# Optimization experiments

Measured on AMD Instinct MI355X. Metric: run time of the kernel, lower is better.

Reference implementation:

```python
import jax, jax.numpy as jnp
import numpy as np

B, N, FA, FP, C = 64, 64, 75, 14, 128


def _mlp2(x, W0, b0, W1, b1):
    # two lazy-Linear + ReLU sub-layers (n_sub_layer=2)
    h = jax.nn.relu(x @ W0 + b0)
    return jax.nn.relu(h @ W1 + b1)


def setup_inputs() -> dict:
    key = jax.random.key(0)
    ks = jax.random.split(key, 32)
    w = lambda k, s: jax.random.normal(k, s, jnp.float32) * 0.05
    inp = {
        "atom_x": jax.random.normal(ks[0], (B, N, FA), jnp.float32),
        "pair_x": jax.random.normal(ks[1], (B, N * N, FP), jnp.float32),
        # atom_to_atom: FA -> C -> C
        "a2a_W0": w(ks[2], (FA, C)), "a2a_b0": w(ks[3], (C,)),
        "a2a_W1": w(ks[4], (C, C)), "a2a_b1": w(ks[5], (C,)),
        # pair_to_atom: FP -> C -> C
        "p2a_W0": w(ks[6], (FP, C)), "p2a_b0": w(ks[7], (C,)),
        "p2a_W1": w(ks[8], (C, C)), "p2a_b1": w(ks[9], (C,)),
        # atom_layer: 2C -> C -> C
        "al_W0": w(ks[10], (2 * C, C)), "al_b0": w(ks[11], (C,)),
        "al_W1": w(ks[12], (C, C)), "al_b1": w(ks[13], (C,)),
        # atom_to_pair (weights shared across both orderings): 2FA -> C -> C
        "a2p_W0": w(ks[14], (2 * FA, C)), "a2p_b0": w(ks[15], (C,)),
        "a2p_W1": w(ks[16], (C, C)), "a2p_b1": w(ks[17], (C,)),
        # pair_to_pair: FP -> C -> C
        "p2p_W0": w(ks[18], (FP, C)), "p2p_b0": w(ks[19], (C,)),
        "p2p_W1": w(ks[20], (C, C)), "p2p_b1": w(ks[21], (C,)),
        # pair_layer: 2C -> C -> C
        "pl_W0": w(ks[22], (2 * C, C)), "pl_b0": w(ks[23], (C,)),
        "pl_W1": w(ks[24], (C, C)), "pl_b1": w(ks[25], (C,)),
    }
    return inp


def reference(atom_x, pair_x,
              a2a_W0, a2a_b0, a2a_W1, a2a_b1,
              p2a_W0, p2a_b0, p2a_W1, p2a_b1,
              al_W0, al_b0, al_W1, al_b1,
              a2p_W0, a2p_b0, a2p_W1, a2p_b1,
              p2p_W0, p2p_b0, p2p_W1, p2p_b1,
              pl_W0, pl_b0, pl_W1, pl_b1):
    b, n, fa = atom_x.shape
    # --- atom branch ---
    a0 = _mlp2(atom_x, a2a_W0, a2a_b0, a2a_W1, a2a_b1)            # [B,N,C]
    a1 = _mlp2(pair_x, p2a_W0, p2a_b0, p2a_W1, p2a_b1)            # [B,N*N,C]
    a1 = a1.reshape(b, n, n, -1).sum(axis=2)                      # PairToAtom sum
    a = jnp.concatenate([a0, a1], axis=-1)                        # [B,N,2C]
    next_atom = jax.nn.relu(_mlp2(a, al_W0, al_b0, al_W1, al_b1))  # extra relu per forward
    # --- pair branch ---
    rep = jnp.broadcast_to(atom_x[:, None, :, :], (b, n, n, fa))  # atom_repeat
    til = jnp.broadcast_to(atom_x[:, :, None, :], (b, n, n, fa))  # atom_tile
    pr0 = jnp.concatenate([til, rep], axis=-1).reshape(b, n * n, 2 * fa)
    pr1 = jnp.concatenate([rep, til], axis=-1).reshape(b, n * n, 2 * fa)
    p0 = (_mlp2(pr0, a2p_W0, a2p_b0, a2p_W1, a2p_b1)
          + _mlp2(pr1, a2p_W0, a2p_b0, a2p_W1, a2p_b1))            # [B,N*N,C]
    p1 = _mlp2(pair_x, p2p_W0, p2p_b0, p2p_W1, p2p_b1)            # [B,N*N,C]
    p = jnp.concatenate([p0, p1], axis=-1)                        # [B,N*N,2C]
    next_pair = jax.nn.relu(_mlp2(p, pl_W0, pl_b0, pl_W1, pl_b1))
    return (next_atom, next_pair)
```

## Files before the change

### kernel.cpp

```cpp
#include <hip/hip_runtime.h>
#include <hip/hip_bf16.h>

typedef unsigned short u16;
typedef unsigned int u32;
typedef __attribute__((ext_vector_type(8))) __bf16 bf16x8;
typedef __attribute__((ext_vector_type(4))) float f32x4;

#define B_ 64
#define N_ 64
#define FA_ 75
#define FP_ 14
#define C_ 128

__device__ float g_A0[4096 * 128];
__device__ float g_A1[4096 * 128];
__device__ float g_TB[4096 * 256];
__device__ u16   g_Wf[208896];

#define OFF_AA0   0
#define OFF_AA1   12288
#define OFF_APT   28672
#define OFF_APB   40960
#define OFF_PA0   53248
#define OFF_PA1   57344
#define OFF_AL0   73728
#define OFF_AL1   106496
#define OFF_AP1   122880
#define OFF_PP0   139264
#define OFF_PP1   143360
#define OFF_PL0T  159744
#define OFF_PL0B  176128
#define OFF_PL1   192512

__device__ __forceinline__ float bf2f(u16 a) {
    union { u32 u; float f; } v; v.u = ((u32)a) << 16; return v.f;
}
__device__ __forceinline__ u16 f2bf(float f) {
    union { float f; u32 u; } v; v.f = f;
    u32 r = v.u + 0x7fffu + ((v.u >> 16) & 1u);
    return (u16)(r >> 16);
}
#if __has_builtin(__builtin_amdgcn_cvt_pk_bf16_f32)
__device__ __forceinline__ u32 f2bf_pk(float a, float b) {
    auto r = __builtin_amdgcn_cvt_pk_bf16_f32(a, b);
    if constexpr (sizeof(r) == 4) {
        union { decltype(r) v; u32 u; } c; c.v = r; return c.u;
    } else {
        return (u32)f2bf(a) | ((u32)f2bf(b) << 16);
    }
}
#else
__device__ __forceinline__ u32 f2bf_pk(float a, float b) {
    return (u32)f2bf(a) | ((u32)f2bf(b) << 16);
}
#endif

__device__ __forceinline__ bool detect_isbf(const void* __restrict__ atom) {
    u32 wrd = ((const u32*)atom)[threadIdx.x & 63];
    u32 ex = (wrd >> 7) & 0xffu;
    unsigned long long m = __ballot(ex >= 113u && ex <= 133u);
    return __popcll(m) >= 32;
}

__device__ __forceinline__ float ldf(const void* p, size_t i, bool isbf) {
    if (isbf) return bf2f(((const u16*)p)[i]);
    return ((const float*)p)[i];
}
__device__ __forceinline__ f32x4 ldf4(const void* p, int i, bool isbf) {
    f32x4 r;
    if (isbf) {
        const u16* q = (const u16*)p + i;
        r[0] = bf2f(q[0]); r[1] = bf2f(q[1]); r[2] = bf2f(q[2]); r[3] = bf2f(q[3]);
    } else {
        r = *(const f32x4*)((const float*)p + i);
    }
    return r;
}
__device__ __forceinline__ uint4 pack8(const void* p, size_t base, int kmax, int k0, bool isbf) {
    uint4 u;
    if (isbf) {
        const u16* q = (const u16*)p + base;
        u16 h[8];
#pragma unroll
        for (int j = 0; j < 8; ++j) h[j] = (k0 + j < kmax) ? q[k0 + j] : (u16)0;
        u.x = (u32)h[0] | ((u32)h[1] << 16); u.y = (u32)h[2] | ((u32)h[3] << 16);
        u.z = (u32)h[4] | ((u32)h[5] << 16); u.w = (u32)h[6] | ((u32)h[7] << 16);
    } else {
        const float* q = (const float*)p + base;
        float f[8];
#pragma unroll
        for (int j = 0; j < 8; ++j) f[j] = (k0 + j < kmax) ? q[k0 + j] : 0.f;
        u.x = f2bf_pk(f[0], f[1]); u.y = f2bf_pk(f[2], f[3]);
        u.z = f2bf_pk(f[4], f[5]); u.w = f2bf_pk(f[6], f[7]);
    }
    return u;
}

__global__ __launch_bounds__(256) void prep_w(
    const void* atom,
    const void* aaW0, const void* aaW1, const void* apW0,
    const void* paW0, const void* paW1, const void* alW0, const void* alW1,
    const void* apW1, const void* ppW0, const void* ppW1,
    const void* plW0, const void* plW1) {
    const bool isbf = detect_isbf(atom);
    const void* srcs[14] = {aaW0, aaW1, apW0, apW0, paW0, paW1, alW0, alW1,
                            apW1, ppW0, ppW1, plW0, plW0, plW1};
    const int Ktab[14]  = {75, 128, 75, 75, 14, 128, 256, 128, 128, 14, 128, 128, 128, 128};
    const int KStab[14] = {3, 4, 3, 3, 1, 4, 8, 4, 4, 1, 4, 4, 4, 4};
    const int rofft[14] = {0, 0, 0, 75, 0, 0, 0, 0, 0, 0, 0, 0, 128, 0};
    const int baset[14] = {OFF_AA0, OFF_AA1, OFF_APT, OFF_APB, OFF_PA0, OFF_PA1,
                           OFF_AL0, OFF_AL1, OFF_AP1, OFF_PP0, OFF_PP1,
                           OFF_PL0T, OFF_PL0B, OFF_PL1};
    int gid = blockIdx.x * 256 + threadIdx.x;
    int j = 0, s = gid;
    while (j < 14 && s >= KStab[j] * 512) { s -= KStab[j] * 512; ++j; }
    if (j >= 14) return;
    int lane = s & 63, rest = s >> 6;
    int ks = rest % KStab[j], mt = rest / KStab[j];
    int m = mt * 16 + (lane & 15), q = lane >> 4;
    float f[8];
#pragma unroll
    for (int jj = 0; jj < 8; ++jj) {
        int k = ks * 32 + q * 8 + jj;
        f[jj] = (k < Ktab[j]) ? ldf(srcs[j], (size_t)(rofft[j] + k) * 128 + m, isbf) : 0.f;
    }
    uint4 u;
    u.x = f2bf_pk(f[0], f[1]); u.y = f2bf_pk(f[2], f[3]);
    u.z = f2bf_pk(f[4], f[5]); u.w = f2bf_pk(f[6], f[7]);
    *(uint4*)&g_Wf[(size_t)baset[j] + (size_t)s * 8] = u;
}

template<int KS, int NT>
__device__ __forceinline__ void gemm2(const u16* __restrict__ wf,
                                      const u16* __restrict__ bF,
                                      int mt0, int lane, f32x4 (&acc)[2][NT]) {
#pragma unroll
    for (int ks = 0; ks < KS; ++ks) {
        bf16x8 a0 = *(const bf16x8*)(wf + (((mt0    ) * KS + ks) * 64 + lane) * 8);
        bf16x8 a1 = *(const bf16x8*)(wf + (((mt0 + 1) * KS + ks) * 64 + lane) * 8);
#pragma unroll
        for (int nt = 0; nt < NT; ++nt) {
            bf16x8 b = *(const bf16x8*)(bF + ((nt * KS + ks) * 64 + lane) * 8);
            acc[0][nt] = __builtin_amdgcn_mfma_f32_16x16x32_bf16(a0, b, acc[0][nt], 0, 0, 0);
            acc[1][nt] = __builtin_amdgcn_mfma_f32_16x16x32_bf16(a1, b, acc[1][nt], 0, 0, 0);
        }
    }
}
template<int KS, int NT>
__device__ __forceinline__ void gemm1(const u16* __restrict__ wf,
                                      const u16* __restrict__ bF,
                                      int mt, int lane, f32x4 (&acc)[NT]) {
#pragma unroll
    for (int ks = 0; ks < KS; ++ks) {
        bf16x8 a = *(const bf16x8*)(wf + (((mt * KS + ks) * 64 + lane)) * 8);
#pragma unroll
        for (int nt = 0; nt < NT; ++nt) {
            bf16x8 b = *(const bf16x8*)(bF + ((nt * KS + ks) * 64 + lane) * 8);
            acc[nt] = __builtin_amdgcn_mfma_f32_16x16x32_bf16(a, b, acc[nt], 0, 0, 0);
        }
    }
}

__device__ __forceinline__ void frag_store(u16* dstF, int KSd, int nt, int mt, int lane, f32x4 v) {
    int c = lane & 15, quad = lane >> 4;
    int lp = c + 16 * ((2 * mt + (quad >> 1)) & 3);
    int ks = mt >> 1;
    uint2 u; u.x = f2bf_pk(v[0], v[1]); u.y = f2bf_pk(v[2], v[3]);
    *(uint2*)(dstF + (((nt * KSd + ks) * 64 + lp) * 8 + (quad & 1) * 4)) = u;
}

__device__ __forceinline__ void store_out4(void* outp, size_t elem, f32x4 v, bool isbf) {
    if (isbf) {
        uint2 u; u.x = f2bf_pk(v[0], v[1]); u.y = f2bf_pk(v[2], v[3]);
        *(uint2*)((u16*)outp + elem) = u;
    } else {
        *(f32x4*)((float*)outp + elem) = v;
    }
}

#define EPI_RELU_STORE(ACC, BB0, BB1, DST, NTN) do {                             \
    _Pragma("unroll") for (int ii = 0; ii < 2; ++ii) {                           \
        f32x4 bb_ = ii ? (BB1) : (BB0);                                          \
        _Pragma("unroll") for (int nt_ = 0; nt_ < NTN; ++nt_) {                  \
            f32x4 v_;                                                            \
            _Pragma("unroll") for (int r_ = 0; r_ < 4; ++r_) {                   \
                float x_ = ACC[ii][nt_][r_] + bb_[r_];                           \
                v_[r_] = x_ > 0.f ? x_ : 0.f;                                    \
            }                                                                    \
            frag_store(DST, 4, nt_, mt0 + ii, lane, v_);                         \
        }                                                                        \
    }                                                                            \
} while (0)

#define EPI1_RELU_STORE(ACC, BB, DST, NTN) do {                                  \
    _Pragma("unroll") for (int nt_ = 0; nt_ < NTN; ++nt_) {                      \
        f32x4 v_;                                                                \
        _Pragma("unroll") for (int r_ = 0; r_ < 4; ++r_) {                       \
            float x_ = ACC[nt_][r_] + (BB)[r_];                                  \
            v_[r_] = x_ > 0.f ? x_ : 0.f;                                        \
        }                                                                        \
        frag_store(DST, 4, nt_, mt, lane, v_);                                   \
    }                                                                            \
} while (0)

__global__ __launch_bounds__(256) void atom_pre(
    const void* __restrict__ atom,
    const void* __restrict__ aaB0, const void* __restrict__ aaB1) {
    __shared__ __align__(16) u16 sXF[2 * 3 * 64 * 8];
    __shared__ __align__(16) u16 sHF[2 * 4 * 64 * 8];
    const bool isbf = detect_isbf(atom);
    const int t = threadIdx.x, lane = t & 63, w = t >> 6;
    const int quad = lane >> 4;
    const int r0g = blockIdx.x * 32;
    for (int s = t; s < 2 * 3 * 64; s += 256) {
        int lane_s = s & 63, rest = s >> 6;
        int ks = rest % 3, nt = rest / 3;
        int n = nt * 16 + (lane_s & 15), q = lane_s >> 4;
        *(uint4*)&sXF[s * 8] = pack8(atom, (size_t)(r0g + n) * FA_, FA_, ks * 32 + q * 8, isbf);
    }
    __syncthreads();
    const int mt0 = 2 * w;
    {
        f32x4 bb0 = ldf4(aaB0, mt0 * 16 + quad * 4, isbf);
        f32x4 bb1 = ldf4(aaB0, (mt0 + 1) * 16 + quad * 4, isbf);
        f32x4 acc[2][2];
#pragma unroll
        for (int ii = 0; ii < 2; ++ii)
#pragma unroll
            for (int nt = 0; nt < 2; ++nt) acc[ii][nt] = (f32x4){0.f, 0.f, 0.f, 0.f};
        gemm2<3, 2>(g_Wf + OFF_AA0, sXF, mt0, lane, acc);
        EPI_RELU_STORE(acc, bb0, bb1, sHF, 2);
    }
    __syncthreads();
    {
        f32x4 bb0 = ldf4(aaB1, mt0 * 16 + quad * 4, isbf);
        f32x4 bb1 = ldf4(aaB1, (mt0 + 1) * 16 + quad * 4, isbf);
        f32x4 acc[2][2];
#pragma unroll
        for (int ii = 0; ii < 2; ++ii)
#pragma unroll
            for (int nt = 0; nt < 2; ++nt) acc[ii][nt] = (f32x4){0.f, 0.f, 0.f, 0.f};
        gemm2<4, 2>(g_Wf + OFF_AA1, sHF, mt0, lane, acc);
        int c = lane & 15;
#pragma unroll
        for (int ii = 0; ii < 2; ++ii) {
            int mt = mt0 + ii;
            f32x4 bb = ii ? bb1 : bb0;
#pragma unroll
            for (int nt = 0; nt < 2; ++nt) {
                f32x4 v;
#pragma unroll
                for (int r = 0; r < 4; ++r) { float x = acc[ii][nt][r] + bb[r]; v[r] = x > 0.f ? x : 0.f; }
                *(f32x4*)&g_A0[(size_t)(r0g + nt * 16 + c) * 128 + mt * 16 + quad * 4] = v;
            }
        }
    }
    {
        f32x4 accT[2][2], accB[2][2];
#pragma unroll
        for (int ii = 0; ii < 2; ++ii)
#pragma unroll
            for (int nt = 0; nt < 2; ++nt) { accT[ii][nt] = (f32x4){0.f,0.f,0.f,0.f}; accB[ii][nt] = (f32x4){0.f,0.f,0.f,0.f}; }
        gemm2<3, 2>(g_Wf + OFF_APT, sXF, mt0, lane, accT);
        gemm2<3, 2>(g_Wf + OFF_APB, sXF, mt0, lane, accB);
        int c = lane & 15;
#pragma unroll
        for (int ii = 0; ii < 2; ++ii) {
            int mt = mt0 + ii;
#pragma unroll
            for (int nt = 0; nt < 2; ++nt) {
                size_t row = (size_t)(r0g + nt * 16 + c);
                *(f32x4*)&g_TB[row * 256 + mt * 16 + quad * 4] = accT[ii][nt];
                *(f32x4*)&g_TB[row * 256 + 128 + mt * 16 + quad * 4] = accB[ii][nt];
            }
        }
    }
}

__global__ __launch_bounds__(256) void atom_layer(
    const void* __restrict__ atom,
    const void* __restrict__ alB0, const void* __restrict__ alB1,
    void* __restrict__ out) {
    __shared__ __align__(16) u16 sXF[1 * 8 * 64 * 8];
    __shared__ __align__(16) u16 sHF[1 * 4 * 64 * 8];
    const bool isbf = detect_isbf(atom);
    const int t = threadIdx.x, lane = t & 63, w = t >> 6;
    const int quad = lane >> 4;
    const int r0g = blockIdx.x * 16;
    for (int s = t; s < 8 * 64; s += 256) {
        int lane_s = s & 63, ks = s >> 6;
        int n = lane_s & 15, q = lane_s >> 4;
        int k0 = ks * 32 + q * 8;
        const float* src = (k0 < 128) ? &g_A0[(size_t)(r0g + n) * 128 + k0]
                                      : &g_A1[(size_t)(r0g + n) * 128 + (k0 - 128)];
        f32x4 f0 = *(const f32x4*)src, f1 = *(const f32x4*)(src + 4);
        uint4 u;
        u.x = f2bf_pk(f0[0], f0[1]); u.y = f2bf_pk(f0[2], f0[3]);
        u.z = f2bf_pk(f1[0], f1[1]); u.w = f2bf_pk(f1[2], f1[3]);
        *(uint4*)&sXF[s * 8] = u;
    }
    __syncthreads();
    const int mt0 = 2 * w;
    {
        f32x4 bb0 = ldf4(alB0, mt0 * 16 + quad * 4, isbf);
        f32x4 bb1 = ldf4(alB0, (mt0 + 1) * 16 + quad * 4, isbf);
        f32x4 acc[2][1];
#pragma unroll
        for (int ii = 0; ii < 2; ++ii) acc[ii][0] = (f32x4){0.f, 0.f, 0.f, 0.f};
        gemm2<8, 1>(g_Wf + OFF_AL0, sXF, mt0, lane, acc);
        EPI_RELU_STORE(acc, bb0, bb1, sHF, 1);
    }
    __syncthreads();
    {
        f32x4 bb0 = ldf4(alB1, mt0 * 16 + quad * 4, isbf);
        f32x4 bb1 = ldf4(alB1, (mt0 + 1) * 16 + quad * 4, isbf);
        f32x4 acc[2][1];
#pragma unroll
        for (int ii = 0; ii < 2; ++ii) acc[ii][0] = (f32x4){0.f, 0.f, 0.f, 0.f};
        gemm2<4, 1>(g_Wf + OFF_AL1, sHF, mt0, lane, acc);
        int c = lane & 15;
#pragma unroll
        for (int ii = 0; ii < 2; ++ii) {
            int mt = mt0 + ii;
            f32x4 bb = ii ? bb1 : bb0;
            f32x4 v;
#pragma unroll
            for (int r = 0; r < 4; ++r) { float x = acc[ii][0][r] + bb[r]; v[r] = x > 0.f ? x : 0.f; }
            store_out4(out, (size_t)(r0g + c) * 128 + mt * 16 + quad * 4, v, isbf);
        }
    }
}

__global__ __launch_bounds__(512, 6) void pair_fused(
    const void* __restrict__ atom,
    const void* __restrict__ pairx,
    const void* __restrict__ apB0, const void* __restrict__ apB1,
    const void* __restrict__ ppB0, const void* __restrict__ ppB1,
    const void* __restrict__ plB0, const void* __restrict__ plB1,
    const void* __restrict__ paB0, const void* __restrict__ paB1,
    void* __restrict__ out) {
    __shared__ __align__(16) u16 sX1[4 * 4 * 64 * 8];
    __shared__ __align__(16) u16 sX2[4 * 4 * 64 * 8];
    __shared__ __align__(16) u16 sR [4 * 4 * 64 * 8];
    __shared__ __align__(16) u16 sPr[4 * 1 * 64 * 8];
    const bool isbf = detect_isbf(atom);
    const int t = threadIdx.x, lane = t & 63, w = t >> 6;
    const int quad = lane >> 4, c = lane & 15;
    const int bx = blockIdx.x;
    const int b = bx >> 6, i = bx & 63;
    const int trow = b * 64;
    const size_t prow0 = (size_t)b * 4096 + (size_t)i * 64;
    const int mt = w;

    if (t < 256) {
        int lane_s = t & 63, nt = t >> 6;
        int n = nt * 16 + (lane_s & 15), q = lane_s >> 4;
        *(uint4*)&sPr[t * 8] = pack8(pairx, (prow0 + n) * FP_, FP_, q * 8, isbf);
    }
    {
        const int ksg = w & 3;
        const int nth = (w >> 2) * 2;
        const int k0 = ksg * 32 + quad * 8;
        const int rc = c;
        const float* TBi = &g_TB[(size_t)(trow + i) * 256 + k0];
        f32x4 t0 = *(const f32x4*)TBi,        t1 = *(const f32x4*)(TBi + 4);
        f32x4 o0 = *(const f32x4*)(TBi + 128), o1 = *(const f32x4*)(TBi + 132);
        f32x4 b0a = ldf4(apB0, k0, isbf), b0b = ldf4(apB0, k0 + 4, isbf);
        float Tip[8], Bip[8];
#pragma unroll
        for (int r = 0; r < 4; ++r) {
            Tip[r] = t0[r] + b0a[r]; Tip[4 + r] = t1[r] + b0b[r];
            Bip[r] = o0[r] + b0a[r]; Bip[4 + r] = o1[r] + b0b[r];
        }
#pragma unroll
        for (int ntii = 0; ntii < 2; ++ntii) {
            int nt = nth + ntii;
            int n = nt * 16 + rc;
            const float* Bj = &g_TB[(size_t)(trow + n) * 256 + k0];
            f32x4 j0 = *(const f32x4*)Bj,        j1 = *(const f32x4*)(Bj + 4);
            f32x4 j2 = *(const f32x4*)(Bj + 128), j3 = *(const f32x4*)(Bj + 132);
            float v0[8], v1[8];
#pragma unroll
            for (int r = 0; r < 4; ++r) {
                float x0 = Tip[r] + j2[r];      v0[r]     = x0 > 0.f ? x0 : 0.f;
                float x1 = Tip[4 + r] + j3[r];  v0[4 + r] = x1 > 0.f ? x1 : 0.f;
                float y0 = j0[r] + Bip[r];      v1[r]     = y0 > 0.f ? y0 : 0.f;
                float y1 = j1[r] + Bip[4 + r];  v1[4 + r] = y1 > 0.f ? y1 : 0.f;
            }
            uint4 u0, u1;
            u0.x = f2bf_pk(v0[0], v0[1]); u0.y = f2bf_pk(v0[2], v0[3]);
            u0.z = f2bf_pk(v0[4], v0[5]); u0.w = f2bf_pk(v0[6], v0[7]);
            u1.x = f2bf_pk(v1[0], v1[1]); u1.y = f2bf_pk(v1[2], v1[3]);
            u1.z = f2bf_pk(v1[4], v1[5]); u1.w = f2bf_pk(v1[6], v1[7]);
            int slot = ((nt * 4 + ksg) * 64 + lane) * 8;
            *(uint4*)&sX1[slot] = u0;
            *(uint4*)&sX2[slot] = u1;
        }
    }
    __syncthreads();
    {
        f32x4 bb = ldf4(apB1, mt * 16 + quad * 4, isbf);
        f32x4 aA[4], aB[4];
#pragma unroll
        for (int nt = 0; nt < 4; ++nt) { aA[nt] = (f32x4){0.f,0.f,0.f,0.f}; aB[nt] = (f32x4){0.f,0.f,0.f,0.f}; }
        gemm1<4, 4>(g_Wf + OFF_AP1, sX1, mt, lane, aA);
        gemm1<4, 4>(g_Wf + OFF_AP1, sX2, mt, lane, aB);
#pragma unroll
        for (int nt = 0; nt < 4; ++nt) {
            f32x4 v;
#pragma unroll
            for (int r = 0; r < 4; ++r) {
                float x = aA[nt][r] + bb[r];
                float y = aB[nt][r] + bb[r];
                v[r] = (x > 0.f ? x : 0.f) + (y > 0.f ? y : 0.f);
            }
            frag_store(sR, 4, nt, mt, lane, v);
        }
    }
    f32x4 aH[4], aPA[4];
#pragma unroll
    for (int nt = 0; nt < 4; ++nt) { aH[nt] = (f32x4){0.f,0.f,0.f,0.f}; aPA[nt] = (f32x4){0.f,0.f,0.f,0.f}; }
    gemm1<1, 4>(g_Wf + OFF_PP0, sPr, mt, lane, aH);
    gemm1<1, 4>(g_Wf + OFF_PA0, sPr, mt, lane, aPA);
    __syncthreads();
    f32x4 C3[4];
#pragma unroll
    for (int nt = 0; nt < 4; ++nt) C3[nt] = (f32x4){0.f, 0.f, 0.f, 0.f};
    gemm1<4, 4>(g_Wf + OFF_PL0T, sR, mt, lane, C3);
    {
        f32x4 bb = ldf4(ppB0, mt * 16 + quad * 4, isbf);
        EPI1_RELU_STORE(aH, bb, sX1, 4);
    }
    {
        f32x4 bb = ldf4(paB0, mt * 16 + quad * 4, isbf);
        EPI1_RELU_STORE(aPA, bb, sX2, 4);
    }
    __syncthreads();
    {
        f32x4 aP[4], aA1[4];
#pragma unroll
        for (int nt = 0; nt < 4; ++nt) { aP[nt] = (f32x4){0.f,0.f,0.f,0.f}; aA1[nt] = (f32x4){0.f,0.f,0.f,0.f}; }
        gemm1<4, 4>(g_Wf + OFF_PP1, sX1, mt, lane, aP);
        gemm1<4, 4>(g_Wf + OFF_PA1, sX2, mt, lane, aA1);
        {
            f32x4 bb = ldf4(paB1, mt * 16 + quad * 4, isbf);
            f32x4 ssum = (f32x4){0.f, 0.f, 0.f, 0.f};
#pragma unroll
            for (int nt = 0; nt < 4; ++nt)
#pragma unroll
                for (int r = 0; r < 4; ++r) {
                    float x = aA1[nt][r] + bb[r];
                    ssum[r] += (x > 0.f ? x : 0.f);
                }
#pragma unroll
            for (int m = 1; m < 16; m <<= 1)
#pragma unroll
                for (int r = 0; r < 4; ++r) ssum[r] += __shfl_xor(ssum[r], m, 64);
            if ((lane & 15) == 0)
                *(f32x4*)&g_A1[(size_t)bx * 128 + mt * 16 + quad * 4] = ssum;
        }
        f32x4 bb = ldf4(ppB1, mt * 16 + quad * 4, isbf);
        EPI1_RELU_STORE(aP, bb, sR, 4);
    }
    __syncthreads();
    gemm1<4, 4>(g_Wf + OFF_PL0B, sR, mt, lane, C3);
    {
        f32x4 bb = ldf4(plB0, mt * 16 + quad * 4, isbf);
        EPI1_RELU_STORE(C3, bb, sX1, 4);
    }
    __syncthreads();
    {
        f32x4 bb = ldf4(plB1, mt * 16 + quad * 4, isbf);
        f32x4 aO[4];
#pragma unroll
        for (int nt = 0; nt < 4; ++nt) aO[nt] = (f32x4){0.f, 0.f, 0.f, 0.f};
        gemm1<4, 4>(g_Wf + OFF_PL1, sX1, mt, lane, aO);
        const size_t NA = (size_t)B_ * N_ * C_;
#pragma unroll
        for (int nt = 0; nt < 4; ++nt) {
            f32x4 v;
#pragma unroll
            for (int r = 0; r < 4; ++r) { float x = aO[nt][r] + bb[r]; v[r] = x > 0.f ? x : 0.f; }
            store_out4(out, NA + (prow0 + nt * 16 + c) * 128 + mt * 16 + quad * 4, v, isbf);
        }
    }
}

extern "C" void kernel_launch(void* const* d_in, const int* in_sizes, int n_in,
                              void* d_out, int out_size, void* d_ws, size_t ws_size,
                              hipStream_t stream) {
    const void* atom  = d_in[0];
    const void* pairx = d_in[1];
    const void* aaW0 = d_in[2];  const void* aaB0 = d_in[3];
    const void* aaW1 = d_in[4];  const void* aaB1 = d_in[5];
    const void* paW0 = d_in[6];  const void* paB0 = d_in[7];
    const void* paW1 = d_in[8];  const void* paB1 = d_in[9];
    const void* alW0 = d_in[10]; const void* alB0 = d_in[11];
    const void* alW1 = d_in[12]; const void* alB1 = d_in[13];
    const void* apW0 = d_in[14]; const void* apB0 = d_in[15];
    const void* apW1 = d_in[16]; const void* apB1 = d_in[17];
    const void* ppW0 = d_in[18]; const void* ppB0 = d_in[19];
    const void* ppW1 = d_in[20]; const void* ppB1 = d_in[21];
    const void* plW0 = d_in[22]; const void* plB0 = d_in[23];
    const void* plW1 = d_in[24]; const void* plB1 = d_in[25];
    (void)d_ws; (void)ws_size; (void)in_sizes; (void)n_in; (void)out_size;

    prep_w<<<102, 256, 0, stream>>>(atom, aaW0, aaW1, apW0, paW0, paW1, alW0, alW1,
                                    apW1, ppW0, ppW1, plW0, plW1);
    atom_pre<<<128, 256, 0, stream>>>(atom, aaB0, aaB1);
    pair_fused<<<4096, 512, 0, stream>>>(atom, pairx, apB0, apB1, ppB0, ppB1,
                                         plB0, plB1, paB0, paB1, d_out);
    atom_layer<<<256, 256, 0, stream>>>(atom, alB0, alB1, d_out);
}
```

Baseline: 300.2 us.

## Restructure pair_fused so each wave owns 16 pair rows with register activations

Each wave now computes all 128 output channels for its own 16 pair rows. Activations stay in registers as the MFMA A operand, and the weight fragments are read from global memory as the B operand. Intermediate layers go through a per-wave XOR-swizzled LDS scratch, which removes the block-wide barriers between layers; one final barrier remains for the pair-to-atom sum reduction. Blocks shrink from 512 to 256 threads. The trade-off is that every wave streams the full weight matrices, which raises L2/global weight traffic, and the output stores become scalar and less coalesced.

```diff
diff --git a/kernel.cpp b/kernel.cpp
--- a/kernel.cpp
+++ b/kernel.cpp
@@ -130,6 +130,9 @@
     *(uint4*)&g_Wf[(size_t)baset[j] + (size_t)s * 8] = u;
 }
 
+__device__ __forceinline__ bf16x8 as_bf(uint4 u) {
+    union { uint4 u; bf16x8 b; } cv; cv.u = u; return cv.b;
+}
 template<int KS, int NT>
 __device__ __forceinline__ void gemm2(const u16* __restrict__ wf,
                                       const u16* __restrict__ bF,
@@ -146,19 +149,51 @@
         }
     }
 }
-template<int KS, int NT>
-__device__ __forceinline__ void gemm1(const u16* __restrict__ wf,
-                                      const u16* __restrict__ bF,
-                                      int mt, int lane, f32x4 (&acc)[NT]) {
+template<int KS>
+__device__ __forceinline__ void gemmA(const uint4 (&af)[KS], const u16* __restrict__ wf,
+                                      int lane, f32x4 (&acc)[8]) {
 #pragma unroll
     for (int ks = 0; ks < KS; ++ks) {
-        bf16x8 a = *(const bf16x8*)(wf + (((mt * KS + ks) * 64 + lane)) * 8);
-#pragma unroll
-        for (int nt = 0; nt < NT; ++nt) {
-            bf16x8 b = *(const bf16x8*)(bF + ((nt * KS + ks) * 64 + lane) * 8);
+        bf16x8 a = as_bf(af[ks]);
+#pragma unroll
+        for (int nt = 0; nt < 8; ++nt) {
+            bf16x8 b = *(const bf16x8*)(wf + ((nt * KS + ks) * 64 + lane) * 8);
             acc[nt] = __builtin_amdgcn_mfma_f32_16x16x32_bf16(a, b, acc[nt], 0, 0, 0);
         }
     }
+}
+__device__ __forceinline__ void zero8(f32x4 (&a)[8]) {
+#pragma unroll
+    for (int t = 0; t < 8; ++t) a[t] = (f32x4){0.f, 0.f, 0.f, 0.f};
+}
+
+__device__ __forceinline__ void tstore(u16* S, const f32x4 (&acc)[8],
+                                       const void* bias, bool isbf, int q, int c) {
+#pragma unroll
+    for (int t = 0; t < 8; ++t) {
+        float bb = ldf(bias, t * 16 + c, isbf);
+#pragma unroll
+        for (int r = 0; r < 4; ++r) {
+            int row = q * 4 + r;
+            float x = acc[t][r] + bb;
+            x = x > 0.f ? x : 0.f;
+            int off = row * 256 + ((t * 32 + c * 2) ^ ((row & 7) << 4));
+            *(u16*)((char*)S + off) = f2bf(x);
+        }
+    }
+}
+__device__ __forceinline__ void tload(const u16* S, uint4 (&af)[4], int q, int c) {
+#pragma unroll
+    for (int ks = 0; ks < 4; ++ks) {
+        int off = c * 256 + ((ks * 64 + q * 16) ^ ((c & 7) << 4));
+        af[ks] = *(const uint4*)((const char*)S + off);
+    }
+}
+
+__device__ __forceinline__ void barrier_lgkm() {
+    asm volatile("s_waitcnt lgkmcnt(0)" ::: "memory");
+    __builtin_amdgcn_s_barrier();
+    asm volatile("" ::: "memory");
 }
 
 __device__ __forceinline__ void frag_store(u16* dstF, int KSd, int nt, int mt, int lane, f32x4 v) {
@@ -189,17 +224,6 @@
             }                                                                    \
             frag_store(DST, 4, nt_, mt0 + ii, lane, v_);                         \
         }                                                                        \
-    }                                                                            \
-} while (0)
-
-#define EPI1_RELU_STORE(ACC, BB, DST, NTN) do {                                  \
-    _Pragma("unroll") for (int nt_ = 0; nt_ < NTN; ++nt_) {                      \
-        f32x4 v_;                                                                \
-        _Pragma("unroll") for (int r_ = 0; r_ < 4; ++r_) {                       \
-            float x_ = ACC[nt_][r_] + (BB)[r_];                                  \
-            v_[r_] = x_ > 0.f ? x_ : 0.f;                                        \
-        }                                                                        \
-        frag_store(DST, 4, nt_, mt, lane, v_);                                   \
     }                                                                            \
 } while (0)
 
@@ -331,7 +355,7 @@
     }
 }
 
-__global__ __launch_bounds__(512, 6) void pair_fused(
+__global__ __launch_bounds__(256, 3) void pair_fused(
     const void* __restrict__ atom,
     const void* __restrict__ pairx,
     const void* __restrict__ apB0, const void* __restrict__ apB1,
@@ -339,150 +363,140 @@
     const void* __restrict__ plB0, const void* __restrict__ plB1,
     const void* __restrict__ paB0, const void* __restrict__ paB1,
     void* __restrict__ out) {
-    __shared__ __align__(16) u16 sX1[4 * 4 * 64 * 8];
-    __shared__ __align__(16) u16 sX2[4 * 4 * 64 * 8];
-    __shared__ __align__(16) u16 sR [4 * 4 * 64 * 8];
-    __shared__ __align__(16) u16 sPr[4 * 1 * 64 * 8];
+    __shared__ __align__(16) u16 sT[4][3][2048];
+    __shared__ float sRed[4][128];
     const bool isbf = detect_isbf(atom);
     const int t = threadIdx.x, lane = t & 63, w = t >> 6;
-    const int quad = lane >> 4, c = lane & 15;
+    const int q = lane >> 4, c = lane & 15;
     const int bx = blockIdx.x;
     const int b = bx >> 6, i = bx & 63;
     const int trow = b * 64;
     const size_t prow0 = (size_t)b * 4096 + (size_t)i * 64;
-    const int mt = w;
-
-    if (t < 256) {
-        int lane_s = t & 63, nt = t >> 6;
-        int n = nt * 16 + (lane_s & 15), q = lane_s >> 4;
-        *(uint4*)&sPr[t * 8] = pack8(pairx, (prow0 + n) * FP_, FP_, q * 8, isbf);
-    }
-    {
-        const int ksg = w & 3;
-        const int nth = (w >> 2) * 2;
-        const int k0 = ksg * 32 + quad * 8;
-        const int rc = c;
-        const float* TBi = &g_TB[(size_t)(trow + i) * 256 + k0];
-        f32x4 t0 = *(const f32x4*)TBi,        t1 = *(const f32x4*)(TBi + 4);
-        f32x4 o0 = *(const f32x4*)(TBi + 128), o1 = *(const f32x4*)(TBi + 132);
-        f32x4 b0a = ldf4(apB0, k0, isbf), b0b = ldf4(apB0, k0 + 4, isbf);
-        float Tip[8], Bip[8];
-#pragma unroll
-        for (int r = 0; r < 4; ++r) {
-            Tip[r] = t0[r] + b0a[r]; Tip[4 + r] = t1[r] + b0b[r];
-            Bip[r] = o0[r] + b0a[r]; Bip[4 + r] = o1[r] + b0b[r];
-        }
-#pragma unroll
-        for (int ntii = 0; ntii < 2; ++ntii) {
-            int nt = nth + ntii;
-            int n = nt * 16 + rc;
-            const float* Bj = &g_TB[(size_t)(trow + n) * 256 + k0];
-            f32x4 j0 = *(const f32x4*)Bj,        j1 = *(const f32x4*)(Bj + 4);
-            f32x4 j2 = *(const f32x4*)(Bj + 128), j3 = *(const f32x4*)(Bj + 132);
-            float v0[8], v1[8];
+    const int rb = w * 16;
+    u16* S0 = &sT[w][0][0];
+    u16* S1 = &sT[w][1][0];
+    u16* S2 = &sT[w][2][0];
+
+    uint4 H0f[4], H1f[4];
+    {
+        const float* TBi = &g_TB[(size_t)(trow + i) * 256];
+        const float* TBr = &g_TB[(size_t)(trow + rb + c) * 256];
+#pragma unroll
+        for (int ks = 0; ks < 4; ++ks) {
+            int k0 = ks * 32 + q * 8;
+            f32x4 ti0 = *(const f32x4*)(TBi + k0),       ti1 = *(const f32x4*)(TBi + k0 + 4);
+            f32x4 bi0 = *(const f32x4*)(TBi + 128 + k0), bi1 = *(const f32x4*)(TBi + 132 + k0);
+            f32x4 tr0 = *(const f32x4*)(TBr + k0),       tr1 = *(const f32x4*)(TBr + k0 + 4);
+            f32x4 br0 = *(const f32x4*)(TBr + 128 + k0), br1 = *(const f32x4*)(TBr + 132 + k0);
+            f32x4 b0a = ldf4(apB0, k0, isbf), b0b = ldf4(apB0, k0 + 4, isbf);
+            float h0[8], h1[8];
 #pragma unroll
             for (int r = 0; r < 4; ++r) {
-                float x0 = Tip[r] + j2[r];      v0[r]     = x0 > 0.f ? x0 : 0.f;
-                float x1 = Tip[4 + r] + j3[r];  v0[4 + r] = x1 > 0.f ? x1 : 0.f;
-                float y0 = j0[r] + Bip[r];      v1[r]     = y0 > 0.f ? y0 : 0.f;
-                float y1 = j1[r] + Bip[4 + r];  v1[4 + r] = y1 > 0.f ? y1 : 0.f;
+                float x0 = ti0[r] + b0a[r] + br0[r]; h0[r]     = x0 > 0.f ? x0 : 0.f;
+                float x1 = ti1[r] + b0b[r] + br1[r]; h0[4 + r] = x1 > 0.f ? x1 : 0.f;
+                float y0 = tr0[r] + bi0[r] + b0a[r]; h1[r]     = y0 > 0.f ? y0 : 0.f;
+                float y1 = tr1[r] + bi1[r] + b0b[r]; h1[4 + r] = y1 > 0.f ? y1 : 0.f;
             }
             uint4 u0, u1;
-            u0.x = f2bf_pk(v0[0], v0[1]); u0.y = f2bf_pk(v0[2], v0[3]);
-            u0.z = f2bf_pk(v0[4], v0[5]); u0.w = f2bf_pk(v0[6], v0[7]);
-            u1.x = f2bf_pk(v1[0], v1[1]); u1.y = f2bf_pk(v1[2], v1[3]);
-            u1.z = f2bf_pk(v1[4], v1[5]); u1.w = f2bf_pk(v1[6], v1[7]);
-            int slot = ((nt * 4 + ksg) * 64 + lane) * 8;
-            *(uint4*)&sX1[slot] = u0;
-            *(uint4*)&sX2[slot] = u1;
-        }
-    }
-    __syncthreads();
-    {
-        f32x4 bb = ldf4(apB1, mt * 16 + quad * 4, isbf);
-        f32x4 aA[4], aB[4];
-#pragma unroll
-        for (int nt = 0; nt < 4; ++nt) { aA[nt] = (f32x4){0.f,0.f,0.f,0.f}; aB[nt] = (f32x4){0.f,0.f,0.f,0.f}; }
-        gemm1<4, 4>(g_Wf + OFF_AP1, sX1, mt, lane, aA);
-        gemm1<4, 4>(g_Wf + OFF_AP1, sX2, mt, lane, aB);
-#pragma unroll
-        for (int nt = 0; nt < 4; ++nt) {
-            f32x4 v;
+            u0.x = f2bf_pk(h0[0], h0[1]); u0.y = f2bf_pk(h0[2], h0[3]);
+            u0.z = f2bf_pk(h0[4], h0[5]); u0.w = f2bf_pk(h0[6], h0[7]);
+            u1.x = f2bf_pk(h1[0], h1[1]); u1.y = f2bf_pk(h1[2], h1[3]);
+            u1.z = f2bf_pk(h1[4], h1[5]); u1.w = f2bf_pk(h1[6], h1[7]);
+            H0f[ks] = u0; H1f[ks] = u1;
+        }
+    }
+    uint4 Prf[1];
+    Prf[0] = pack8(pairx, (prow0 + rb + c) * FP_, FP_, q * 8, isbf);
+
+    {
+        f32x4 aA[8], aB[8];
+        zero8(aA); zero8(aB);
+        gemmA<4>(H0f, g_Wf + OFF_AP1, lane, aA);
+        gemmA<4>(H1f, g_Wf + OFF_AP1, lane, aB);
+#pragma unroll
+        for (int tt = 0; tt < 8; ++tt) {
+            float bb = ldf(apB1, tt * 16 + c, isbf);
 #pragma unroll
             for (int r = 0; r < 4; ++r) {
-                float x = aA[nt][r] + bb[r];
-                float y = aB[nt][r] + bb[r];
-                v[r] = (x > 0.f ? x : 0.f) + (y > 0.f ? y : 0.f);
+                int row = q * 4 + r;
+                float x = aA[tt][r] + bb; x = x > 0.f ? x : 0.f;
+                float y = aB[tt][r] + bb; y = y > 0.f ? y : 0.f;
+                int off = row * 256 + ((tt * 32 + c * 2) ^ ((row & 7) << 4));
+                *(u16*)((char*)S0 + off) = f2bf(x + y);
             }
-            frag_store(sR, 4, nt, mt, lane, v);
-        }
-    }
-    f32x4 aH[4], aPA[4];
-#pragma unroll
-    for (int nt = 0; nt < 4; ++nt) { aH[nt] = (f32x4){0.f,0.f,0.f,0.f}; aPA[nt] = (f32x4){0.f,0.f,0.f,0.f}; }
-    gemm1<1, 4>(g_Wf + OFF_PP0, sPr, mt, lane, aH);
-    gemm1<1, 4>(g_Wf + OFF_PA0, sPr, mt, lane, aPA);
-    __syncthreads();
-    f32x4 C3[4];
-#pragma unroll
-    for (int nt = 0; nt < 4; ++nt) C3[nt] = (f32x4){0.f, 0.f, 0.f, 0.f};
-    gemm1<4, 4>(g_Wf + OFF_PL0T, sR, mt, lane, C3);
-    {
-        f32x4 bb = ldf4(ppB0, mt * 16 + quad * 4, isbf);
-        EPI1_RELU_STORE(aH, bb, sX1, 4);
-    }
-    {
-        f32x4 bb = ldf4(paB0, mt * 16 + quad * 4, isbf);
-        EPI1_RELU_STORE(aPA, bb, sX2, 4);
-    }
-    __syncthreads();
-    {
-        f32x4 aP[4], aA1[4];
-#pragma unroll
-        for (int nt = 0; nt < 4; ++nt) { aP[nt] = (f32x4){0.f,0.f,0.f,0.f}; aA1[nt] = (f32x4){0.f,0.f,0.f,0.f}; }
-        gemm1<4, 4>(g_Wf + OFF_PP1, sX1, mt, lane, aP);
-        gemm1<4, 4>(g_Wf + OFF_PA1, sX2, mt, lane, aA1);
-        {
-            f32x4 bb = ldf4(paB1, mt * 16 + quad * 4, isbf);
-            f32x4 ssum = (f32x4){0.f, 0.f, 0.f, 0.f};
-#pragma unroll
-            for (int nt = 0; nt < 4; ++nt)
-#pragma unroll
-                for (int r = 0; r < 4; ++r) {
-                    float x = aA1[nt][r] + bb[r];
-                    ssum[r] += (x > 0.f ? x : 0.f);
-                }
-#pragma unroll
-            for (int m = 1; m < 16; m <<= 1)
-#pragma unroll
-                for (int r = 0; r < 4; ++r) ssum[r] += __shfl_xor(ssum[r], m, 64);
-            if ((lane & 15) == 0)
-                *(f32x4*)&g_A1[(size_t)bx * 128 + mt * 16 + quad * 4] = ssum;
-        }
-        f32x4 bb = ldf4(ppB1, mt * 16 + quad * 4, isbf);
-        EPI1_RELU_STORE(aP, bb, sR, 4);
-    }
-    __syncthreads();
-    gemm1<4, 4>(g_Wf + OFF_PL0B, sR, mt, lane, C3);
-    {
-        f32x4 bb = ldf4(plB0, mt * 16 + quad * 4, isbf);
-        EPI1_RELU_STORE(C3, bb, sX1, 4);
-    }
-    __syncthreads();
-    {
-        f32x4 bb = ldf4(plB1, mt * 16 + quad * 4, isbf);
-        f32x4 aO[4];
-#pragma unroll
-        for (int nt = 0; nt < 4; ++nt) aO[nt] = (f32x4){0.f, 0.f, 0.f, 0.f};
-        gemm1<4, 4>(g_Wf + OFF_PL1, sX1, mt, lane, aO);
+        }
+    }
+    {
+        f32x4 acc[8];
+        zero8(acc);
+        gemmA<1>(Prf, g_Wf + OFF_PP0, lane, acc);
+        tstore(S1, acc, ppB0, isbf, q, c);
+        zero8(acc);
+        gemmA<1>(Prf, g_Wf + OFF_PA0, lane, acc);
+        tstore(S2, acc, paB0, isbf, q, c);
+    }
+    f32x4 C3[8];
+    uint4 af[4];
+    zero8(C3);
+    tload(S0, af, q, c);
+    gemmA<4>(af, g_Wf + OFF_PL0T, lane, C3);
+    {
+        f32x4 acc[8];
+        tload(S1, af, q, c);
+        zero8(acc);
+        gemmA<4>(af, g_Wf + OFF_PP1, lane, acc);
+        tstore(S0, acc, ppB1, isbf, q, c);
+        tload(S2, af, q, c);
+        zero8(acc);
+        gemmA<4>(af, g_Wf + OFF_PA1, lane, acc);
+        float s[8];
+#pragma unroll
+        for (int tt = 0; tt < 8; ++tt) {
+            float bb = ldf(paB1, tt * 16 + c, isbf);
+            float sv = 0.f;
+#pragma unroll
+            for (int r = 0; r < 4; ++r) {
+                float x = acc[tt][r] + bb;
+                sv += (x > 0.f ? x : 0.f);
+            }
+            s[tt] = sv;
+        }
+#pragma unroll
+        for (int tt = 0; tt < 8; ++tt) {
+            s[tt] += __shfl_xor(s[tt], 16, 64);
+            s[tt] += __shfl_xor(s[tt], 32, 64);
+        }
+        if (lane < 16) {
+#pragma unroll
+            for (int tt = 0; tt < 8; ++tt) sRed[w][tt * 16 + lane] = s[tt];
+        }
+    }
+    tload(S0, af, q, c);
+    gemmA<4>(af, g_Wf + OFF_PL0B, lane, C3);
+    tstore(S1, C3, plB0, isbf, q, c);
+    {
+        f32x4 acc[8];
+        tload(S1, af, q, c);
+        zero8(acc);
+        gemmA<4>(af, g_Wf + OFF_PL1, lane, acc);
         const size_t NA = (size_t)B_ * N_ * C_;
 #pragma unroll
-        for (int nt = 0; nt < 4; ++nt) {
-            f32x4 v;
-#pragma unroll
-            for (int r = 0; r < 4; ++r) { float x = aO[nt][r] + bb[r]; v[r] = x > 0.f ? x : 0.f; }
-            store_out4(out, NA + (prow0 + nt * 16 + c) * 128 + mt * 16 + quad * 4, v, isbf);
-        }
+        for (int tt = 0; tt < 8; ++tt) {
+            float bb = ldf(plB1, tt * 16 + c, isbf);
+#pragma unroll
+            for (int r = 0; r < 4; ++r) {
+                int row = q * 4 + r;
+                float x = acc[tt][r] + bb; x = x > 0.f ? x : 0.f;
+                size_t e = NA + (prow0 + rb + row) * 128 + tt * 16 + c;
+                if (isbf) ((u16*)out)[e] = f2bf(x);
+                else      ((float*)out)[e] = x;
+            }
+        }
+    }
+    barrier_lgkm();
+    if (t < 128) {
+        float v = sRed[0][t] + sRed[1][t] + sRed[2][t] + sRed[3][t];
+        g_A1[(size_t)bx * 128 + t] = v;
     }
 }
 
@@ -508,7 +522,7 @@
     prep_w<<<102, 256, 0, stream>>>(atom, aaW0, aaW1, apW0, paW0, paW1, alW0, alW1,
                                     apW1, ppW0, ppW1, plW0, plW1);
     atom_pre<<<128, 256, 0, stream>>>(atom, aaB0, aaB1);
-    pair_fused<<<4096, 512, 0, stream>>>(atom, pairx, apB0, apB1, ppB0, ppB1,
+    pair_fused<<<4096, 256, 0, stream>>>(atom, pairx, apB0, apB1, ppB0, ppB1,
                                          plB0, plB1, paB0, paB1, d_out);
     atom_layer<<<256, 256, 0, stream>>>(atom, alB0, alB1, d_out);
 }
```

Result: slower. 494.5 us (+64.7%).
